# Optimization experiments

Measured on AMD Instinct MI355X. Metric: run time of the kernel, lower is better.

## Reference

```python
import jax, jax.numpy as jnp
import numpy as np

B, C_IN, C_OUT = 32, 64, 128
K_SIZE, STRIDE, PAD, H = 3, 1, 1, 56
H_OUT = (H + 2 * PAD - K_SIZE) // STRIDE + 1


def setup_inputs() -> dict:
    key = jax.random.key(0)
    kx, kw = jax.random.split(key)
    x = jax.random.normal(kx, (B, C_IN, H, H), dtype=jnp.float32)
    # kaiming_uniform-ish init for K of shape [kh, kw, C_in, C_out]
    fan_in = K_SIZE * C_IN * C_OUT  # torch fan_in for this layout (dim1 * receptive field)
    bound = np.sqrt(6.0 / fan_in).astype(np.float32)
    K = jax.random.uniform(kw, (K_SIZE, K_SIZE, C_IN, C_OUT), dtype=jnp.float32,
                           minval=-bound, maxval=bound)
    return {"x": x, "K": K}


def reference(x, K):
    # Faithful to the torch code INCLUDING its mismatched flatten orders:
    #   patch flattened as (C_in, kh, kw); K flattened as (kh, kw, C_in).
    xp = jnp.pad(x, ((0, 0), (0, 0), (PAD, PAD), (PAD, PAD)))
    end = (H_OUT - 1) * STRIDE + 1
    # patches[b, c, di, dj, i, j] = xp[b, c, i*stride+di, j*stride+dj]
    rows = []
    for di in range(K_SIZE):
        cols = []
        for dj in range(K_SIZE):
            cols.append(xp[:, :, di:di + end:STRIDE, dj:dj + end:STRIDE])  # [B,C,Ho,Wo]
        rows.append(jnp.stack(cols, axis=2))  # [B,C,kw,Ho,Wo]
    patches = jnp.stack(rows, axis=2)  # [B, C, kh, kw, Ho, Wo]
    # flatten patch in (C, kh, kw) order -> [B, Ho, Wo, C*kh*kw]
    p = patches.transpose(0, 4, 5, 1, 2, 3).reshape(B, H_OUT, H_OUT, -1)
    # K flattened in (kh, kw, C) order, exactly as K.view(-1, out_channels)
    Kf = K.reshape(-1, C_OUT)  # [kh*kw*C_in, C_out]
    out = p @ Kf  # [B, Ho, Wo, C_out]
    return out.transpose(0, 3, 1, 2)  # [B, C_out, Ho, Wo]
```

## Files before the change

### kernel.cpp

```cpp
#include <hip/hip_runtime.h>
#include <hip/hip_bf16.h>
#include <stdint.h>


#define B_   32
#define CIN  64
#define COUT 128
#define H_   56
#define HP   58
#define F_   576

typedef __attribute__((ext_vector_type(8))) short bf16x8;
typedef __attribute__((ext_vector_type(4))) float f32x4;

#define XP_ELEMS (B_*HP*HP*CIN)
#define XP_SLACK 4096
#define XP_TOTAL (XP_ELEMS + XP_SLACK)
#define WG_ELEMS (COUT*F_)
#define WS_NEEDED ((size_t)(XP_TOTAL + WG_ELEMS) * 2)

#define NROW   (B_*HP)
#define NWBLK  (WG_ELEMS/256)

#define A_ALLOC 74240
#define LDS_TOT (A_ALLOC + 64*F_*2)

__device__ __forceinline__ int aswz(int tot) {
  return (tot & ~127) | ((tot & 127) ^ (((tot >> 7) & 7) << 4));
}

__global__ __launch_bounds__(256) void prep_all(const float* __restrict__ x,
                                                const float* __restrict__ K,
                                                __hip_bfloat16* __restrict__ xpT,
                                                __hip_bfloat16* __restrict__ WgT) {
  const int id = blockIdx.x;
  const int t  = threadIdx.x;

  if (id > NROW) {
    int n = (id - (NROW + 1))*256 + t;
    int co = n / F_, g = n % F_;
    int di = g / 192, dj = (g % 192) / 64, c = g & 63;
    int f  = c*9 + di*3 + dj;
    int kh = f / 192, kw = (f % 192) / 64, cc = f & 63;
    WgT[n] = __float2bfloat16(K[(((size_t)kh*3 + kw)*CIN + cc)*COUT + co]);
    return;
  }
  if (id == NROW) {
    bf16x8 z = (bf16x8)0;
    for (int idx = t; idx < XP_SLACK/8; idx += 256)
      ((bf16x8*)(xpT + XP_ELEMS))[idx] = z;
    return;
  }

  const int b = id / HP, h = id % HP;
  __hip_bfloat16* orow = xpT + (size_t)(b*HP + h) * HP * CIN;
  if (h == 0 || h == HP-1) {
    bf16x8 z = (bf16x8)0;
    for (int idx = t; idx < HP*CIN/8; idx += 256) ((bf16x8*)orow)[idx] = z;
    return;
  }
  __shared__ __align__(16) float scr[CIN*64];
  const float* xrow = x + ((size_t)(b*CIN)*H_ + (h-1)) * H_;
  for (int idx = t; idx < CIN*14; idx += 256) {
    int c = idx / 14, w4 = idx % 14;
    f32x4 v = *(const f32x4*)(xrow + (size_t)c*(H_*H_) + w4*4);
    *(f32x4*)&scr[c*64 + ((w4 + (c >> 3)) & 15)*4] = v;
  }
  __syncthreads();
  for (int idx = t; idx < HP*8; idx += 256) {
    int wp = idx >> 3, cg = (idx & 7) * 8;
    __align__(16) __hip_bfloat16 tmp[8];
    if (wp == 0 || wp == HP-1) {
#pragma unroll
      for (int k2 = 0; k2 < 8; ++k2) tmp[k2] = __float2bfloat16(0.f);
    } else {
      int w = wp - 1, sl = w >> 2, off = w & 3;
#pragma unroll
      for (int k2 = 0; k2 < 8; ++k2) {
        int c = cg + k2;
        tmp[k2] = __float2bfloat16(scr[c*64 + ((sl + (c >> 3)) & 15)*4 + off]);
      }
    }
    *(bf16x8*)(orow + (size_t)wp*CIN + cg) = *(const bf16x8*)tmp;
  }
}

__global__ __launch_bounds__(512, 2) void conv_mfma(
    const __hip_bfloat16* __restrict__ xpT,
    const __hip_bfloat16* __restrict__ WgT,
    float* __restrict__ out) {
  __shared__ __align__(16) char lds[LDS_TOT];
  const int t    = threadIdx.x;
  const int wave = t >> 6;
  const int l    = t & 63;
  const int lr   = l & 15, lq = l >> 4;

  const int bid = blockIdx.x;
  const int swz = (bid & 7) * 56 + (bid >> 3);
  const int bb  = swz / 14;
  const int u   = swz % 14;
  const int i0  = (u >> 1) * 8;
  const int ch  = u & 1;

  f32x4 acc[4][4];
#pragma unroll
  for (int mi = 0; mi < 4; ++mi)
#pragma unroll
    for (int ni = 0; ni < 4; ++ni) acc[mi][ni] = (f32x4)0.f;

  const char* xb = (const char*)xpT + (size_t)(bb*HP + i0) * HP * CIN * 2;
  const char* wh = (const char*)WgT + (size_t)(ch*64)*1152;

#pragma unroll
  for (int s = 0; s < 9; ++s) {
    int o = s*8192 + t*16;
    __builtin_amdgcn_global_load_lds(
        (const __attribute__((address_space(1))) void*)(xb + aswz(o)),
        (__attribute__((address_space(3))) void*)(lds + s*8192 + wave*1024),
        16, 0, 0);
  }
  if (t < 32) {
    int o = 73728 + t*16;
    __builtin_amdgcn_global_load_lds(
        (const __attribute__((address_space(1))) void*)(xb + aswz(o)),
        (__attribute__((address_space(3))) void*)(lds + 73728),
        16, 0, 0);
  }
#pragma unroll
  for (int s = 0; s < 9; ++s) {
    int o  = s*8192 + t*16;
    int co = o / 1152;
    int rb = o - co*1152;
    __builtin_amdgcn_global_load_lds(
        (const __attribute__((address_space(1))) void*)
            (wh + co*1152 + (rb ^ ((co & 7) << 4))),
        (__attribute__((address_space(3))) void*)
            (lds + A_ALLOC + s*8192 + wave*1024),
        16, 0, 0);
  }
  __syncthreads();

#pragma unroll
  for (int hc = 0; hc < 18; ++hc) {
    const int kg  = hc*32;
    const int di  = kg / 192;
    const int rem = kg - di*192;
    bf16x8 a[4], bq[4];
#pragma unroll
    for (int mi = 0; mi < 4; ++mi) {
      int tot = ((wave + di)*HP + mi*16 + lr)*128 + rem*2 + lq*16;
      a[mi] = *(const bf16x8*)(lds + aswz(tot));
    }
    const int kb = hc*64 + lq*16;
#pragma unroll
    for (int ni = 0; ni < 4; ++ni) {
      int co = ni*16 + lr;
      bq[ni] = *(const bf16x8*)(lds + A_ALLOC + co*1152 + (kb ^ ((co & 7) << 4)));
    }
    __builtin_amdgcn_s_setprio(1);
#pragma unroll
    for (int mi = 0; mi < 4; ++mi)
#pragma unroll
      for (int ni = 0; ni < 4; ++ni)
        acc[mi][ni] = __builtin_amdgcn_mfma_f32_16x16x32_bf16(
            a[mi], bq[ni], acc[mi][ni], 0, 0, 0);
    __builtin_amdgcn_s_setprio(0);
  }

  const int i = i0 + wave;
#pragma unroll
  for (int mi = 0; mi < 4; ++mi) {
    int j0 = mi*16 + lq*4;
    if (j0 < H_) {
#pragma unroll
      for (int ni = 0; ni < 4; ++ni) {
        int co = ch*64 + ni*16 + lr;
        float* dst = out + (((size_t)(bb*COUT + co))*H_ + i)*H_ + j0;
        *(f32x4*)dst = acc[mi][ni];
      }
    }
  }
}

__global__ __launch_bounds__(256) void conv_naive(const float* __restrict__ x,
                                                  const float* __restrict__ K,
                                                  float* __restrict__ out) {
  int idx = blockIdx.x*256 + threadIdx.x;
  const int total = B_*COUT*H_*H_;
  if (idx >= total) return;
  int j = idx % H_, i = (idx / H_) % H_, co = (idx / (H_*H_)) % COUT, b = idx / (H_*H_*COUT);
  float s = 0.f;
  for (int c = 0; c < CIN; ++c)
    for (int di = 0; di < 3; ++di) {
      int ii = i + di - 1;
      if (ii < 0 || ii >= H_) continue;
      for (int dj = 0; dj < 3; ++dj) {
        int jj = j + dj - 1;
        if (jj < 0 || jj >= H_) continue;
        int f = c*9 + di*3 + dj;
        int kh = f / 192, kw = (f % 192) / 64, cc = f & 63;
        s += x[(((size_t)b*CIN + c)*H_ + ii)*H_ + jj] *
             K[(((size_t)kh*3 + kw)*CIN + cc)*COUT + co];
      }
    }
  out[idx] = s;
}

extern "C" void kernel_launch(void* const* d_in, const int* in_sizes, int n_in,
                              void* d_out, int out_size, void* d_ws, size_t ws_size,
                              hipStream_t stream) {
  const float* x = (const float*)d_in[0];
  const float* K = (const float*)d_in[1];
  float* out = (float*)d_out;
  if (ws_size >= WS_NEEDED) {
    __hip_bfloat16* xpT = (__hip_bfloat16*)d_ws;
    __hip_bfloat16* WgT = xpT + XP_TOTAL;
    prep_all<<<NROW + 1 + NWBLK, 256, 0, stream>>>(x, K, xpT, WgT);
    conv_mfma<<<B_*14, 512, 0, stream>>>(xpT, WgT, out);
  } else {
    conv_naive<<<(B_*COUT*H_*H_ + 255)/256, 256, 0, stream>>>(x, K, out);
  }
}
```

Baseline: 38.59 us.

## Fuse input padding/transpose/bf16 conversion into the MFMA conv kernel

The separate prep pass that wrote a padded, channel-last bf16 copy of x to workspace is removed. The conv kernel now reads fp32 x rows directly, transposes them through a double-buffered LDS scratch area and writes bf16 into the swizzled A tile. The block-to-tile mapping also changes so the two output-channel halves of a tile are neighbouring blocks. This saves the write and reread of the padded intermediate, but each tile's 10 input rows are now converted twice (once per channel half) with a barrier per row, and the launch-bounds occupancy hint of 2 is dropped.

```diff
diff --git a/kernel.cpp b/kernel.cpp
--- a/kernel.cpp
+++ b/kernel.cpp
@@ -13,14 +13,12 @@
 typedef __attribute__((ext_vector_type(8))) short bf16x8;
 typedef __attribute__((ext_vector_type(4))) float f32x4;
 
-#define XP_ELEMS (B_*HP*HP*CIN)
-#define XP_SLACK 4096
-#define XP_TOTAL (XP_ELEMS + XP_SLACK)
+#define AS1 __attribute__((address_space(1)))
+#define AS3 __attribute__((address_space(3)))
+
 #define WG_ELEMS (COUT*F_)
-#define WS_NEEDED ((size_t)(XP_TOTAL + WG_ELEMS) * 2)
-
-#define NROW   (B_*HP)
-#define NWBLK  (WG_ELEMS/256)
+#define WS_NEEDED ((size_t)WG_ELEMS * 2)
+#define NWBLK (WG_ELEMS/256)
 
 #define A_ALLOC 74240
 #define LDS_TOT (A_ALLOC + 64*F_*2)
@@ -29,64 +27,18 @@
   return (tot & ~127) | ((tot & 127) ^ (((tot >> 7) & 7) << 4));
 }
 
-__global__ __launch_bounds__(256) void prep_all(const float* __restrict__ x,
-                                                const float* __restrict__ K,
-                                                __hip_bfloat16* __restrict__ xpT,
-                                                __hip_bfloat16* __restrict__ WgT) {
-  const int id = blockIdx.x;
-  const int t  = threadIdx.x;
-
-  if (id > NROW) {
-    int n = (id - (NROW + 1))*256 + t;
-    int co = n / F_, g = n % F_;
-    int di = g / 192, dj = (g % 192) / 64, c = g & 63;
-    int f  = c*9 + di*3 + dj;
-    int kh = f / 192, kw = (f % 192) / 64, cc = f & 63;
-    WgT[n] = __float2bfloat16(K[(((size_t)kh*3 + kw)*CIN + cc)*COUT + co]);
-    return;
-  }
-  if (id == NROW) {
-    bf16x8 z = (bf16x8)0;
-    for (int idx = t; idx < XP_SLACK/8; idx += 256)
-      ((bf16x8*)(xpT + XP_ELEMS))[idx] = z;
-    return;
-  }
-
-  const int b = id / HP, h = id % HP;
-  __hip_bfloat16* orow = xpT + (size_t)(b*HP + h) * HP * CIN;
-  if (h == 0 || h == HP-1) {
-    bf16x8 z = (bf16x8)0;
-    for (int idx = t; idx < HP*CIN/8; idx += 256) ((bf16x8*)orow)[idx] = z;
-    return;
-  }
-  __shared__ __align__(16) float scr[CIN*64];
-  const float* xrow = x + ((size_t)(b*CIN)*H_ + (h-1)) * H_;
-  for (int idx = t; idx < CIN*14; idx += 256) {
-    int c = idx / 14, w4 = idx % 14;
-    f32x4 v = *(const f32x4*)(xrow + (size_t)c*(H_*H_) + w4*4);
-    *(f32x4*)&scr[c*64 + ((w4 + (c >> 3)) & 15)*4] = v;
-  }
-  __syncthreads();
-  for (int idx = t; idx < HP*8; idx += 256) {
-    int wp = idx >> 3, cg = (idx & 7) * 8;
-    __align__(16) __hip_bfloat16 tmp[8];
-    if (wp == 0 || wp == HP-1) {
-#pragma unroll
-      for (int k2 = 0; k2 < 8; ++k2) tmp[k2] = __float2bfloat16(0.f);
-    } else {
-      int w = wp - 1, sl = w >> 2, off = w & 3;
-#pragma unroll
-      for (int k2 = 0; k2 < 8; ++k2) {
-        int c = cg + k2;
-        tmp[k2] = __float2bfloat16(scr[c*64 + ((sl + (c >> 3)) & 15)*4 + off]);
-      }
-    }
-    *(bf16x8*)(orow + (size_t)wp*CIN + cg) = *(const bf16x8*)tmp;
-  }
-}
-
-__global__ __launch_bounds__(512, 2) void conv_mfma(
-    const __hip_bfloat16* __restrict__ xpT,
+__global__ __launch_bounds__(256) void prep_w(const float* __restrict__ K,
+                                              __hip_bfloat16* __restrict__ WgT) {
+  int n = blockIdx.x*256 + threadIdx.x;
+  int co = n / F_, g = n % F_;
+  int di = g / 192, dj = (g % 192) / 64, c = g & 63;
+  int f  = c*9 + di*3 + dj;
+  int kh = f / 192, kw = (f % 192) / 64, cc = f & 63;
+  WgT[n] = __float2bfloat16(K[(((size_t)kh*3 + kw)*CIN + cc)*COUT + co]);
+}
+
+__global__ __launch_bounds__(512) void conv_fused(
+    const float* __restrict__ x,
     const __hip_bfloat16* __restrict__ WgT,
     float* __restrict__ out) {
   __shared__ __align__(16) char lds[LDS_TOT];
@@ -97,10 +49,10 @@
 
   const int bid = blockIdx.x;
   const int swz = (bid & 7) * 56 + (bid >> 3);
-  const int bb  = swz / 14;
-  const int u   = swz % 14;
-  const int i0  = (u >> 1) * 8;
-  const int ch  = u & 1;
+  const int v   = swz >> 1;
+  const int ch  = swz & 1;
+  const int bb  = v / 7;
+  const int i0  = (v % 7) * 8;
 
   f32x4 acc[4][4];
 #pragma unroll
@@ -108,35 +60,62 @@
 #pragma unroll
     for (int ni = 0; ni < 4; ++ni) acc[mi][ni] = (f32x4)0.f;
 
-  const char* xb = (const char*)xpT + (size_t)(bb*HP + i0) * HP * CIN * 2;
-  const char* wh = (const char*)WgT + (size_t)(ch*64)*1152;
-
-#pragma unroll
-  for (int s = 0; s < 9; ++s) {
-    int o = s*8192 + t*16;
-    __builtin_amdgcn_global_load_lds(
-        (const __attribute__((address_space(1))) void*)(xb + aswz(o)),
-        (__attribute__((address_space(3))) void*)(lds + s*8192 + wave*1024),
-        16, 0, 0);
-  }
-  if (t < 32) {
-    int o = 73728 + t*16;
-    __builtin_amdgcn_global_load_lds(
-        (const __attribute__((address_space(1))) void*)(xb + aswz(o)),
-        (__attribute__((address_space(3))) void*)(lds + 73728),
-        16, 0, 0);
-  }
+  const float* xb = x + (size_t)bb*CIN*H_*H_;
+  const char*  wh = (const char*)WgT + (size_t)(ch*64)*1152;
+  char* s0 = lds + A_ALLOC;
+  char* s1 = s0 + 16384;
+
+  auto phaseA = [&](int r, char* s) {
+    const int h = i0 + r;
+    if (h == 0 || h == HP-1) return;
+    const float* xr = xb + (size_t)(h-1)*H_;
+    for (int idx = t; idx < CIN*14; idx += 512) {
+      int c = idx / 14, w4 = idx % 14;
+      f32x4 vv = *(const f32x4*)(xr + (size_t)c*(H_*H_) + w4*4);
+      *(f32x4*)(s + c*256 + ((w4 + (c >> 3)) & 15)*16) = vv;
+    }
+  };
+  auto phaseB = [&](int r, const char* s) {
+    const int h = i0 + r;
+    const bool zrow = (h == 0 || h == HP-1);
+    for (int idx = t; idx < HP*8; idx += 512) {
+      int wp = idx >> 3, cg = (idx & 7) * 8;
+      __align__(16) __hip_bfloat16 tmp[8];
+      if (zrow || wp == 0 || wp == HP-1) {
+#pragma unroll
+        for (int k2 = 0; k2 < 8; ++k2) tmp[k2] = __float2bfloat16(0.f);
+      } else {
+        int w = wp - 1, sl = w >> 2, off = w & 3;
+#pragma unroll
+        for (int k2 = 0; k2 < 8; ++k2) {
+          int c = cg + k2;
+          tmp[k2] = __float2bfloat16(
+              *(const float*)(s + c*256 + ((sl + (c >> 3)) & 15)*16 + off*4));
+        }
+      }
+      int tot = (r*HP + wp)*128 + cg*2;
+      *(bf16x8*)(lds + aswz(tot)) = *(const bf16x8*)tmp;
+    }
+  };
+
+  phaseA(0, s0);
+  __syncthreads();
+#pragma unroll
+  for (int r = 0; r < 10; ++r) {
+    const char* sc = (r & 1) ? s1 : s0;
+    phaseB(r, sc);
+    if (r < 9) phaseA(r + 1, (r & 1) ? s0 : s1);
+    __syncthreads();
+  }
+
 #pragma unroll
   for (int s = 0; s < 9; ++s) {
     int o  = s*8192 + t*16;
     int co = o / 1152;
     int rb = o - co*1152;
     __builtin_amdgcn_global_load_lds(
-        (const __attribute__((address_space(1))) void*)
-            (wh + co*1152 + (rb ^ ((co & 7) << 4))),
-        (__attribute__((address_space(3))) void*)
-            (lds + A_ALLOC + s*8192 + wave*1024),
-        16, 0, 0);
+        (const AS1 void*)(wh + co*1152 + (rb ^ ((co & 7) << 4))),
+        (AS3 void*)(lds + A_ALLOC + s*8192 + wave*1024), 16, 0, 0);
   }
   __syncthreads();
 
@@ -213,10 +192,9 @@
   const float* K = (const float*)d_in[1];
   float* out = (float*)d_out;
   if (ws_size >= WS_NEEDED) {
-    __hip_bfloat16* xpT = (__hip_bfloat16*)d_ws;
-    __hip_bfloat16* WgT = xpT + XP_TOTAL;
-    prep_all<<<NROW + 1 + NWBLK, 256, 0, stream>>>(x, K, xpT, WgT);
-    conv_mfma<<<B_*14, 512, 0, stream>>>(xpT, WgT, out);
+    __hip_bfloat16* WgT = (__hip_bfloat16*)d_ws;
+    prep_w<<<NWBLK, 256, 0, stream>>>(K, WgT);
+    conv_fused<<<448, 512, 0, stream>>>(x, WgT, out);
   } else {
     conv_naive<<<(B_*COUT*H_*H_ + 255)/256, 256, 0, stream>>>(x, K, out);
   }
```

After: 46.64 us. 20.9% more time.
